# Kernel tuning notes

Measured on AMD Instinct MI355X. Metric: run time of the kernel, lower is better.

## Reference

```python
import jax, jax.numpy as jnp
import numpy as np

DIM = 1024
HEADS = 16
DIM_HEAD = 64
WINDOW = 256  # sliding window size == block size
NEG = -1e9


def rms_norm(x, gamma, size):
    # F.normalize(x, dim=-1) * sqrt(size) * gamma
    nrm = jnp.sqrt(jnp.sum(x * x, axis=-1, keepdims=True))
    return x / jnp.maximum(nrm, 1e-12) * (size ** 0.5) * gamma


def sliding_window_attention(q, k, v, window):
    # q,k,v: [b, h, S, d]; causal local attention: key j valid iff i-window <= j <= i
    b, h, S, d = q.shape
    Bk = window
    nb = S // Bk
    qb = q.reshape(b, h, nb, Bk, d)
    kb = k.reshape(b, h, nb, Bk, d)
    vb = v.reshape(b, h, nb, Bk, d)
    # previous key/value block (zeros for block 0; masked out below)
    k_prev = jnp.pad(kb, ((0, 0), (0, 0), (1, 0), (0, 0), (0, 0)))[:, :, :nb]
    v_prev = jnp.pad(vb, ((0, 0), (0, 0), (1, 0), (0, 0), (0, 0)))[:, :, :nb]
    kctx = jnp.concatenate([k_prev, kb], axis=3)  # [b,h,nb,2Bk,d]
    vctx = jnp.concatenate([v_prev, vb], axis=3)
    scale = 1.0 / jnp.sqrt(jnp.asarray(d, q.dtype))
    scores = jnp.einsum('bhnqd,bhnkd->bhnqk', qb, kctx) * scale  # [b,h,nb,Bk,2Bk]
    qi = jnp.arange(Bk)[:, None]          # local query index
    kj = jnp.arange(2 * Bk)[None, :]      # local key index (offset -Bk rel to block start)
    diff = Bk + qi - kj                   # global i - j
    base = (diff >= 0) & (diff <= window)  # [Bk, 2Bk]
    blk = jnp.arange(nb)[:, None, None]
    key_exists = ((blk - 1) * Bk + kj[None]) >= 0  # [nb,1,2Bk] -> broadcast
    mask = base[None] & key_exists                 # [nb,Bk,2Bk]
    scores = jnp.where(mask[None, None], scores, NEG)
    attn = jax.nn.softmax(scores, axis=-1)
    out = jnp.einsum('bhnqk,bhnkd->bhnqd', attn, vctx)
    return out.reshape(b, h, S, d)


def setup_inputs() -> dict:
    key = jax.random.key(0)
    ks = jax.random.split(key, 6)
    b, S = 2, 4096
    dim_inner = HEADS * DIM_HEAD
    x = jax.random.normal(ks[0], (b, S, DIM), dtype=jnp.float32)
    gamma = jnp.ones((DIM,), dtype=jnp.float32)
    W_qkv = jax.random.normal(ks[1], (DIM, 3 * dim_inner), dtype=jnp.float32) * 0.02
    W_gates = jax.random.normal(ks[2], (DIM, HEADS), dtype=jnp.float32) * 0.02
    b_gates = jnp.zeros((HEADS,), dtype=jnp.float32)
    W_out = jax.random.normal(ks[3], (dim_inner, DIM), dtype=jnp.float32) * 0.02
    return {"x": x, "gamma": gamma, "W_qkv": W_qkv, "W_gates": W_gates,
            "b_gates": b_gates, "W_out": W_out}


def reference(x, gamma, W_qkv, W_gates, b_gates, W_out):
    b, S, dim = x.shape
    xn = rms_norm(x, gamma, dim)
    qkv = xn @ W_qkv                                    # [b,S,3*h*d]
    qkv = qkv.reshape(b, S, 3, HEADS, DIM_HEAD)
    q, k, v = [jnp.transpose(t, (0, 2, 1, 3)) for t in
               (qkv[:, :, 0], qkv[:, :, 1], qkv[:, :, 2])]  # [b,h,S,d]
    out = sliding_window_attention(q, k, v, WINDOW)      # [b,h,S,d]
    gates = xn @ W_gates + b_gates                       # [b,S,h]
    out = out * jax.nn.sigmoid(jnp.transpose(gates, (0, 2, 1)))[..., None]
    out = jnp.transpose(out, (0, 2, 1, 3)).reshape(b, S, HEADS * DIM_HEAD)
    return out @ W_out
```

## Files before the change

kernel.cpp:

```cpp
#include <hip/hip_runtime.h>
#include <hip/hip_bf16.h>
#include <stdint.h>

typedef __bf16 bf16;
typedef __bf16 bf16x4 __attribute__((ext_vector_type(4)));
typedef __bf16 bf16x8 __attribute__((ext_vector_type(8)));
typedef float f32x4 __attribute__((ext_vector_type(4)));

#define GLOBAL_AS __attribute__((address_space(1)))
#define LDS_AS __attribute__((address_space(3)))

__device__ __forceinline__ void g2lds16(const bf16* g, bf16* l) {
  __builtin_amdgcn_global_load_lds((const GLOBAL_AS void*)g, (LDS_AS void*)l, 16, 0, 0);
}

__global__ __launch_bounds__(256) void rmsnorm_kernel(
    const float* __restrict__ x, const float* __restrict__ gamma,
    bf16* __restrict__ xn) {
  __shared__ float wss[4];
  const int t = threadIdx.x;
  const size_t row = blockIdx.x;
  const float* xr = x + row * 1024;

  float4 xv = *(const float4*)&xr[t * 4];
  float v[4] = {xv.x, xv.y, xv.z, xv.w};
  float ss = v[0]*v[0] + v[1]*v[1] + v[2]*v[2] + v[3]*v[3];
#pragma unroll
  for (int mm = 1; mm < 64; mm <<= 1) ss += __shfl_xor(ss, mm);
  if ((t & 63) == 0) wss[t >> 6] = ss;
  __syncthreads();
  ss = wss[0] + wss[1] + wss[2] + wss[3];
  float inv = 32.0f / sqrtf(fmaxf(ss, 1e-24f));

  float4 gv = *(const float4*)&gamma[t * 4];
  float gvv[4] = {gv.x, gv.y, gv.z, gv.w};
  bf16x4 outv;
#pragma unroll
  for (int i = 0; i < 4; ++i) outv[i] = (bf16)(v[i] * inv * gvv[i]);
  *(bf16x4*)&xn[row * 1024 + t * 4] = outv;
}

__global__ void transpose_f32_bf16(const float* __restrict__ in, bf16* __restrict__ out,
                                   int R, int C) {
  __shared__ bf16 tile[32][33];
  const int tx = threadIdx.x, ty = threadIdx.y;
  const int c0 = blockIdx.x * 32, r0 = blockIdx.y * 32;
#pragma unroll
  for (int i = 0; i < 32; i += 8)
    tile[ty + i][tx] = (bf16)in[(size_t)(r0 + ty + i) * C + c0 + tx];
  __syncthreads();
#pragma unroll
  for (int i = 0; i < 32; i += 8)
    out[(size_t)(c0 + ty + i) * R + r0 + tx] = tile[tx][ty + i];
}

__global__ __launch_bounds__(256) void wg_transpose(const float* __restrict__ Wg,
                                                    bf16* __restrict__ BtAug) {
  int idx = blockIdx.x * 256 + threadIdx.x;
  int n = idx >> 10, k = idx & 1023;
  BtAug[(size_t)(3072 + n) * 1024 + k] = (bf16)Wg[(size_t)k * 16 + n];
}

template <typename OutT>
__global__ __launch_bounds__(256) void gemm_bt_128(
    const bf16* __restrict__ A, const bf16* __restrict__ Bt,
    OutT* __restrict__ C, int M, int N, int K) {
  __shared__ bf16 lA[128 * 64];
  __shared__ bf16 lB[128 * 64];
  const int t = threadIdx.x;
  const int w = t >> 6, lane = t & 63;
  const int col0 = lane & 15, quad = lane >> 4;
  const int m0 = blockIdx.y * 128, n0 = blockIdx.x * 128;
  const int wr = (w >> 1) * 64, wc = (w & 1) * 64;

  const int lrow = t >> 3;
  const int sswz = (((t & 7) ^ (lrow & 7)) << 3);

  f32x4 acc[4][4] = {};

  for (int k0 = 0; k0 < K; k0 += 64) {
    __syncthreads();
#pragma unroll
    for (int c = 0; c < 4; ++c) {
      g2lds16(A  + (size_t)(m0 + c * 32 + lrow) * K + k0 + sswz, &lA[c * 2048 + w * 512]);
      g2lds16(Bt + (size_t)(n0 + c * 32 + lrow) * K + k0 + sswz, &lB[c * 2048 + w * 512]);
    }
    __syncthreads();

#pragma unroll
    for (int kh = 0; kh < 2; ++kh) {
      bf16x8 af[4], bfr[4];
#pragma unroll
      for (int i = 0; i < 4; ++i) {
        int row = wr + i * 16 + col0;
        af[i] = *(const bf16x8*)&lA[row * 64 + (((kh * 4 + quad) ^ (row & 7)) << 3)];
      }
#pragma unroll
      for (int j = 0; j < 4; ++j) {
        int row = wc + j * 16 + col0;
        bfr[j] = *(const bf16x8*)&lB[row * 64 + (((kh * 4 + quad) ^ (row & 7)) << 3)];
      }
#pragma unroll
      for (int i = 0; i < 4; ++i)
#pragma unroll
        for (int j = 0; j < 4; ++j)
          acc[i][j] = __builtin_amdgcn_mfma_f32_16x16x32_bf16(af[i], bfr[j], acc[i][j], 0, 0, 0);
    }
  }

#pragma unroll
  for (int i = 0; i < 4; ++i)
#pragma unroll
    for (int j = 0; j < 4; ++j)
#pragma unroll
      for (int r = 0; r < 4; ++r) {
        int row = m0 + wr + i * 16 + quad * 4 + r;
        int col = n0 + wc + j * 16 + col0;
        C[(size_t)row * N + col] = (OutT)acc[i][j][r];
      }
}

template <typename OutT>
__global__ __launch_bounds__(512, 2) void gemm_bt_256(
    const bf16* __restrict__ A, const bf16* __restrict__ Bt,
    OutT* __restrict__ C, int M, int N, int K) {
  extern __shared__ bf16 lds[];
  bf16* A0 = lds;
  bf16* B0 = lds + 16384;
  bf16* A1 = lds + 32768;
  bf16* B1 = lds + 49152;

  const int t = threadIdx.x;
  const int w = t >> 6, lane = t & 63;
  const int wm = w >> 2, wn = w & 3;
  const int col0 = lane & 15, quad = lane >> 4;
  const int s_sub = lane >> 3;
  const int sswz = (((lane & 7) ^ s_sub) << 3);

  int nwg = gridDim.x * gridDim.y;
  int bid = blockIdx.y * gridDim.x + blockIdx.x;
  int swz = bid;
  if ((nwg & 7) == 0) swz = (bid & 7) * (nwg >> 3) + (bid >> 3);
  const int n0 = (swz % gridDim.x) * 256;
  const int m0 = (swz / gridDim.x) * 256;

  const bf16* Abase = A + (size_t)m0 * (size_t)K;

  auto stageA = [&](int ks, int c, bf16* dstA) {
    int rb = (w < 4) ? (c * 32 + w * 8) : (128 + c * 32 + (w - 4) * 8);
    g2lds16(Abase + (size_t)(rb + s_sub) * K + ks + sswz, dstA + rb * 64);
  };
  auto stageB = [&](int ks, int c, bf16* dstB) {
    int rb = c * 64 + w * 8;
    int gr = n0 + rb + s_sub;
    gr = (gr < N) ? gr : (N - 1);
    g2lds16(Bt + (size_t)gr * (size_t)K + ks + sswz, dstB + rb * 64);
  };

  f32x4 acc[8][4] = {};
  const int NT = K >> 6;
  const int NI = NT >> 1;

#pragma unroll
  for (int c = 0; c < 4; ++c) stageB(0, c, B0);
  stageA(0, 0, A0);
  stageA(0, 1, A0); stageA(0, 2, A0); stageA(0, 3, A0);
  asm volatile("s_waitcnt vmcnt(3)" ::: "memory");
  __builtin_amdgcn_s_barrier();

  for (int i = 0; i < NI; ++i) {
#pragma unroll
    for (int h = 0; h < 2; ++h) {
      bf16* cA = h ? A1 : A0;
      bf16* cB = h ? B1 : B0;
      bf16* nA = h ? A0 : A1;
      bf16* nB = h ? B0 : B1;
      int tn = 2 * i + h + 1;
      int kn = ((tn < NT) ? tn : 0) << 6;

      bf16x8 bv[4][2];
#pragma unroll
      for (int nj = 0; nj < 4; ++nj) {
        int br = wn * 64 + nj * 16 + col0;
#pragma unroll
        for (int ks = 0; ks < 2; ++ks)
          bv[nj][ks] = *(const bf16x8*)&cB[br * 64 + (((ks * 4 + quad) ^ (br & 7)) << 3)];
      }
      {
        bf16x8 af[2][2];
#pragma unroll
        for (int m2 = 0; m2 < 2; ++m2) {
          int ar = wm * 128 + m2 * 16 + col0;
#pragma unroll
          for (int ks = 0; ks < 2; ++ks)
            af[m2][ks] = *(const bf16x8*)&cA[ar * 64 + (((ks * 4 + quad) ^ (ar & 7)) << 3)];
        }
        stageB(kn, 0, nB); stageB(kn, 1, nB);
        __builtin_amdgcn_s_barrier();
        asm volatile("s_waitcnt lgkmcnt(0)" ::: "memory");
        __builtin_amdgcn_s_setprio(1);
#pragma unroll
        for (int ks = 0; ks < 2; ++ks)
#pragma unroll
          for (int m2 = 0; m2 < 2; ++m2)
#pragma unroll
            for (int nj = 0; nj < 4; ++nj)
              acc[m2][nj] = __builtin_amdgcn_mfma_f32_16x16x32_bf16(
                  af[m2][ks], bv[nj][ks], acc[m2][nj], 0, 0, 0);
        __builtin_amdgcn_s_setprio(0);
        asm volatile("s_waitcnt vmcnt(4)" ::: "memory");
        __builtin_amdgcn_s_barrier();
      }

#pragma unroll
      for (int p = 1; p < 4; ++p) {
        bf16x8 af[2][2];
#pragma unroll
        for (int m2 = 0; m2 < 2; ++m2) {
          int ar = wm * 128 + (p * 2 + m2) * 16 + col0;
#pragma unroll
          for (int ks = 0; ks < 2; ++ks)
            af[m2][ks] = *(const bf16x8*)&cA[ar * 64 + (((ks * 4 + quad) ^ (ar & 7)) << 3)];
        }
        if (p == 1)      { stageB(kn, 2, nB); stageB(kn, 3, nB); stageA(kn, 0, nA); }
        else if (p == 2) { stageA(kn, 1, nA); stageA(kn, 2, nA); }
        else             { stageA(kn, 3, nA); }
        __builtin_amdgcn_s_barrier();
        asm volatile("s_waitcnt lgkmcnt(0)" ::: "memory");
        __builtin_amdgcn_s_setprio(1);
#pragma unroll
        for (int ks = 0; ks < 2; ++ks)
#pragma unroll
          for (int m2 = 0; m2 < 2; ++m2)
#pragma unroll
            for (int nj = 0; nj < 4; ++nj)
              acc[p * 2 + m2][nj] = __builtin_amdgcn_mfma_f32_16x16x32_bf16(
                  af[m2][ks], bv[nj][ks], acc[p * 2 + m2][nj], 0, 0, 0);
        __builtin_amdgcn_s_setprio(0);
        if (p == 1)      asm volatile("s_waitcnt vmcnt(6)" ::: "memory");
        else if (p == 2) asm volatile("s_waitcnt vmcnt(7)" ::: "memory");
        else             asm volatile("s_waitcnt vmcnt(3)" ::: "memory");
        __builtin_amdgcn_s_barrier();
      }
    }
  }
  asm volatile("s_waitcnt vmcnt(0)" ::: "memory");

#pragma unroll
  for (int mi = 0; mi < 8; ++mi)
#pragma unroll
    for (int nj = 0; nj < 4; ++nj) {
      int col = n0 + wn * 64 + nj * 16 + col0;
      if (col < N) {
        size_t base = (size_t)(m0 + wm * 128 + mi * 16 + quad * 4) * N + col;
#pragma unroll
        for (int r = 0; r < 4; ++r)
          C[base + (size_t)r * N] = (OutT)acc[mi][nj][r];
      }
    }
}

#define NEG_BIG -1e30f
__global__ __launch_bounds__(256) void attn_kernel(
    const bf16* __restrict__ qkv, const float* __restrict__ bg,
    bf16* __restrict__ attnO) {
  __shared__ bf16 lQ[64 * 64];
  __shared__ bf16 lKV[320 * 64];
  __shared__ bf16 lP[4 * 16 * 32];

  const int t = threadIdx.x;
  const int w = t >> 6, lane = t & 63;
  const int col0 = lane & 15, quad = lane >> 4;

  const int blk = blockIdx.x;
  const int g = blk & 63;
  const int h = (blk >> 6) & 15;
  const int bb = blk >> 10;
  const int qs = g * 64;

  const size_t rs = 3200;
  const bf16* qbase = qkv + ((size_t)bb * 4096) * rs + h * 64;

  for (int c = t; c < 64 * 8; c += 256) {
    int row = c >> 3, ck = c & 7;
    *(uint4*)&lQ[row * 64 + ((ck ^ (row & 7)) << 3)] =
        *(const uint4*)(qbase + (size_t)(qs + row) * rs + ck * 8);
  }
  for (int c = t; c < 320 * 8; c += 256) {
    int row = c >> 3, ck = c & 7;
    int j = qs - 256 + row;
    uint4 val = {0, 0, 0, 0};
    if (j >= 0) val = *(const uint4*)(qbase + 1024 + (size_t)j * rs + ck * 8);
    *(uint4*)&lKV[row * 64 + ((ck ^ (row & 7)) << 3)] = val;
  }
  __syncthreads();

  const int qrow = w * 16 + col0;
  bf16x8 a0 = *(const bf16x8*)&lQ[qrow * 64 + ((quad ^ (qrow & 7)) << 3)];
  bf16x8 a1 = *(const bf16x8*)&lQ[qrow * 64 + (((4 + quad) ^ (qrow & 7)) << 3)];
  f32x4 s[20];
#pragma unroll
  for (int kt = 0; kt < 20; ++kt) {
    int krow = kt * 16 + col0;
    bf16x8 b0 = *(const bf16x8*)&lKV[krow * 64 + ((quad ^ (krow & 7)) << 3)];
    bf16x8 b1 = *(const bf16x8*)&lKV[krow * 64 + (((4 + quad) ^ (krow & 7)) << 3)];
    f32x4 z = {};
    z = __builtin_amdgcn_mfma_f32_16x16x32_bf16(a0, b0, z, 0, 0, 0);
    z = __builtin_amdgcn_mfma_f32_16x16x32_bf16(a1, b1, z, 0, 0, 0);
    s[kt] = z;
  }
  __syncthreads();

  {
    const int jl = t & 31, dg = t >> 5;
#pragma unroll
    for (int cc = 0; cc < 10; ++cc) {
      int j = qs - 256 + cc * 32 + jl;
      bf16 tmp[8];
      if (j >= 0) {
        *(uint4*)tmp = *(const uint4*)(qbase + 2048 + (size_t)j * rs + dg * 8);
      } else {
#pragma unroll
        for (int d2 = 0; d2 < 8; ++d2) tmp[d2] = (bf16)0.f;
      }
      int ck = cc * 4 + (jl >> 3);
      int wi = jl & 7;
#pragma unroll
      for (int d2 = 0; d2 < 8; ++d2) {
        int d = dg * 8 + d2;
        lKV[d * 320 + ((ck ^ (d & 7)) << 3) + wi] = tmp[d2];
      }
    }
  }

  float mrow[4] = {NEG_BIG, NEG_BIG, NEG_BIG, NEG_BIG};
  float lrow[4] = {0, 0, 0, 0};
#pragma unroll
  for (int kt = 0; kt < 20; ++kt) {
    int c = kt * 16 + col0;
#pragma unroll
    for (int r = 0; r < 4; ++r) {
      int ql = w * 16 + quad * 4 + r;
      bool valid = (c >= ql) && (c <= ql + 256) && (qs - 256 + c >= 0);
      float sv = valid ? s[kt][r] * 0.125f : NEG_BIG;
      s[kt][r] = sv;
      mrow[r] = fmaxf(mrow[r], sv);
    }
  }
#pragma unroll
  for (int mm = 1; mm < 16; mm <<= 1)
#pragma unroll
    for (int r = 0; r < 4; ++r) mrow[r] = fmaxf(mrow[r], __shfl_xor(mrow[r], mm));
#pragma unroll
  for (int kt = 0; kt < 20; ++kt)
#pragma unroll
    for (int r = 0; r < 4; ++r) {
      float p = __expf(s[kt][r] - mrow[r]);
      s[kt][r] = p;
      lrow[r] += p;
    }
#pragma unroll
  for (int mm = 1; mm < 16; mm <<= 1)
#pragma unroll
    for (int r = 0; r < 4; ++r) lrow[r] += __shfl_xor(lrow[r], mm);

  __syncthreads();

  f32x4 o[4] = {};
  bf16* pw = &lP[w * 512];
#pragma unroll
  for (int kc = 0; kc < 10; ++kc) {
#pragma unroll
    for (int r = 0; r < 4; ++r) {
      pw[(quad * 4 + r) * 32 + col0]      = (bf16)s[2 * kc][r];
      pw[(quad * 4 + r) * 32 + 16 + col0] = (bf16)s[2 * kc + 1][r];
    }
    asm volatile("s_waitcnt lgkmcnt(0)" ::: "memory");
    bf16x8 pa = *(const bf16x8*)&pw[col0 * 32 + quad * 8];
#pragma unroll
    for (int n = 0; n < 4; ++n) {
      int d = n * 16 + col0;
      bf16x8 bvv = *(const bf16x8*)&lKV[d * 320 + (((kc * 4 + quad) ^ (d & 7)) << 3)];
      o[n] = __builtin_amdgcn_mfma_f32_16x16x32_bf16(pa, bvv, o[n], 0, 0, 0);
    }
  }

  const bf16* gbase = qkv + ((size_t)bb * 4096) * rs + 3072 + h;
  const float bgh = bg[h];
#pragma unroll
  for (int r = 0; r < 4; ++r) {
    int ql = w * 16 + quad * 4 + r;
    int srow = qs + ql;
    float logit = (float)gbase[(size_t)srow * rs] + bgh;
    float gate = 1.f / (1.f + __expf(-logit));
    float scale = gate / lrow[r];
#pragma unroll
    for (int n = 0; n < 4; ++n)
      attnO[((size_t)bb * 4096 + srow) * 1024 + h * 64 + n * 16 + col0] =
          (bf16)(o[n][r] * scale);
  }
}

extern "C" void kernel_launch(void* const* d_in, const int* in_sizes, int n_in,
                              void* d_out, int out_size, void* d_ws, size_t ws_size,
                              hipStream_t stream) {
  const float *x = nullptr, *gamma = nullptr, *Wqkv = nullptr,
              *Wg = nullptr, *bg = nullptr, *Wout = nullptr;
  for (int i = 0; i < n_in; ++i) {
    switch (in_sizes[i]) {
      case 8388608: x     = (const float*)d_in[i]; break;
      case 1024:    gamma = (const float*)d_in[i]; break;
      case 3145728: Wqkv  = (const float*)d_in[i]; break;
      case 16384:   Wg    = (const float*)d_in[i]; break;
      case 16:      bg    = (const float*)d_in[i]; break;
      case 1048576: Wout  = (const float*)d_in[i]; break;
    }
  }
  float* out = (float*)d_out;

  static bool attr_done = false;
  if (!attr_done) {
    hipFuncSetAttribute(reinterpret_cast<const void*>(&gemm_bt_256<bf16>),
                        hipFuncAttributeMaxDynamicSharedMemorySize, 131072);
    attr_done = true;
  }

  char* ws = (char*)d_ws;
  bf16* qkv   = (bf16*)ws;  ws += (size_t)8192 * 3200 * 2;
  bf16* xn    = (bf16*)ws;
  bf16* attnO = (bf16*)ws;  ws += (size_t)8192 * 1024 * 2;
  bf16* BtAug = (bf16*)ws;  ws += (size_t)3200 * 1024 * 2;
  bf16* WoutT = (bf16*)ws;  ws += (size_t)1024 * 1024 * 2;

  hipMemsetAsync(BtAug + (size_t)3088 * 1024, 0, (size_t)112 * 1024 * 2, stream);

  rmsnorm_kernel<<<8192, 256, 0, stream>>>(x, gamma, xn);
  transpose_f32_bf16<<<dim3(3072 / 32, 1024 / 32), dim3(32, 8), 0, stream>>>(Wqkv, BtAug, 1024, 3072);
  wg_transpose<<<64, 256, 0, stream>>>(Wg, BtAug);
  transpose_f32_bf16<<<dim3(1024 / 32, 1024 / 32), dim3(32, 8), 0, stream>>>(Wout, WoutT, 1024, 1024);
  gemm_bt_256<bf16><<<dim3(13, 32), 512, 131072, stream>>>(xn, BtAug, qkv, 8192, 3200, 1024);
  attn_kernel<<<2048, 256, 0, stream>>>(qkv, bg, attnO);
  gemm_bt_128<float><<<dim3(1024 / 128, 8192 / 128), 256, 0, stream>>>(attnO, WoutT, out, 8192, 1024, 1024);
}
```

Baseline: 256.7 us.

## Restructure GEMM prefetch schedule to issue all next-tile loads up front

The GEMM main loop is rescheduled. It now waits for the current B tile and syncs once at the top of each half-step, then issues all eight global-to-LDS loads for the next A/B tile together. It waits for the current A tile before running four unsynchronised MFMA phases. This replaces the old pattern, which spread the next-tile loads across the four phases and put a barrier after each phase. The change cuts barriers per k-step and lets loads stream as a batch, but it drops the fine-grained interleaving of loads with MFMA work. That may expose more memory latency at the top of each step.

```diff
diff --git a/kernel.cpp b/kernel.cpp
--- a/kernel.cpp
+++ b/kernel.cpp
@@ -163,10 +163,8 @@
 
 #pragma unroll
   for (int c = 0; c < 4; ++c) stageB(0, c, B0);
-  stageA(0, 0, A0);
-  stageA(0, 1, A0); stageA(0, 2, A0); stageA(0, 3, A0);
-  asm volatile("s_waitcnt vmcnt(3)" ::: "memory");
-  __builtin_amdgcn_s_barrier();
+#pragma unroll
+  for (int c = 0; c < 4; ++c) stageA(0, c, A0);
 
   for (int i = 0; i < NI; ++i) {
 #pragma unroll
@@ -178,6 +176,9 @@
       int tn = 2 * i + h + 1;
       int kn = ((tn < NT) ? tn : 0) << 6;
 
+      asm volatile("s_waitcnt vmcnt(4)" ::: "memory");
+      __builtin_amdgcn_s_barrier();
+
       bf16x8 bv[4][2];
 #pragma unroll
       for (int nj = 0; nj < 4; ++nj) {
@@ -186,47 +187,23 @@
         for (int ks = 0; ks < 2; ++ks)
           bv[nj][ks] = *(const bf16x8*)&cB[br * 64 + (((ks * 4 + quad) ^ (br & 7)) << 3)];
       }
-      {
+
+      stageB(kn, 0, nB); stageB(kn, 1, nB); stageB(kn, 2, nB); stageB(kn, 3, nB);
+      stageA(kn, 0, nA); stageA(kn, 1, nA); stageA(kn, 2, nA); stageA(kn, 3, nA);
+
+      asm volatile("s_waitcnt vmcnt(8)" ::: "memory");
+      __builtin_amdgcn_s_barrier();
+
+#pragma unroll
+      for (int p = 0; p < 4; ++p) {
         bf16x8 af[2][2];
 #pragma unroll
         for (int m2 = 0; m2 < 2; ++m2) {
-          int ar = wm * 128 + m2 * 16 + col0;
+          int ar = wm * 128 + (p * 2 + m2) * 16 + col0;
 #pragma unroll
           for (int ks = 0; ks < 2; ++ks)
             af[m2][ks] = *(const bf16x8*)&cA[ar * 64 + (((ks * 4 + quad) ^ (ar & 7)) << 3)];
         }
-        stageB(kn, 0, nB); stageB(kn, 1, nB);
-        __builtin_amdgcn_s_barrier();
-        asm volatile("s_waitcnt lgkmcnt(0)" ::: "memory");
-        __builtin_amdgcn_s_setprio(1);
-#pragma unroll
-        for (int ks = 0; ks < 2; ++ks)
-#pragma unroll
-          for (int m2 = 0; m2 < 2; ++m2)
-#pragma unroll
-            for (int nj = 0; nj < 4; ++nj)
-              acc[m2][nj] = __builtin_amdgcn_mfma_f32_16x16x32_bf16(
-                  af[m2][ks], bv[nj][ks], acc[m2][nj], 0, 0, 0);
-        __builtin_amdgcn_s_setprio(0);
-        asm volatile("s_waitcnt vmcnt(4)" ::: "memory");
-        __builtin_amdgcn_s_barrier();
-      }
-
-#pragma unroll
-      for (int p = 1; p < 4; ++p) {
-        bf16x8 af[2][2];
-#pragma unroll
-        for (int m2 = 0; m2 < 2; ++m2) {
-          int ar = wm * 128 + (p * 2 + m2) * 16 + col0;
-#pragma unroll
-          for (int ks = 0; ks < 2; ++ks)
-            af[m2][ks] = *(const bf16x8*)&cA[ar * 64 + (((ks * 4 + quad) ^ (ar & 7)) << 3)];
-        }
-        if (p == 1)      { stageB(kn, 2, nB); stageB(kn, 3, nB); stageA(kn, 0, nA); }
-        else if (p == 2) { stageA(kn, 1, nA); stageA(kn, 2, nA); }
-        else             { stageA(kn, 3, nA); }
-        __builtin_amdgcn_s_barrier();
-        asm volatile("s_waitcnt lgkmcnt(0)" ::: "memory");
         __builtin_amdgcn_s_setprio(1);
 #pragma unroll
         for (int ks = 0; ks < 2; ++ks)
@@ -237,10 +214,6 @@
               acc[p * 2 + m2][nj] = __builtin_amdgcn_mfma_f32_16x16x32_bf16(
                   af[m2][ks], bv[nj][ks], acc[p * 2 + m2][nj], 0, 0, 0);
         __builtin_amdgcn_s_setprio(0);
-        if (p == 1)      asm volatile("s_waitcnt vmcnt(6)" ::: "memory");
-        else if (p == 2) asm volatile("s_waitcnt vmcnt(7)" ::: "memory");
-        else             asm volatile("s_waitcnt vmcnt(3)" ::: "memory");
-        __builtin_amdgcn_s_barrier();
       }
     }
   }
```

Result: no change. 258.1 us (+0.5%).
